# Kernel tuning notes

Measured on AMD Instinct MI355X. Metric: run time of the kernel, lower is better.

## Reference

```python
import jax, jax.numpy as jnp
import numpy as np

B, T, I, U, O, BB = 256, 1024, 64, 256, 64, 128  # batch, seq, input, units, output, backbone_units

def lecun_tanh(x):
    return 1.7159 * jnp.tanh(0.666 * x)

def setup_inputs() -> dict:
    key = jax.random.key(0)
    ks = jax.random.split(key, 13)
    def lin(k, fan_in, fan_out):
        bound = 1.0 / np.sqrt(fan_in)
        kw, kb = jax.random.split(k)
        W = jax.random.uniform(kw, (fan_in, fan_out), jnp.float32, -bound, bound)
        b = jax.random.uniform(kb, (fan_out,), jnp.float32, -bound, bound)
        return W, b
    x = jax.random.normal(ks[0], (B, T, I), jnp.float32)
    W_bb, b_bb = lin(ks[1], I + U, BB)   # backbone Linear
    W_ff1, b_ff1 = lin(ks[2], BB, U)
    W_ff2, b_ff2 = lin(ks[3], BB, U)
    W_ta, b_ta = lin(ks[4], BB, U)       # time_a
    W_tb, b_tb = lin(ks[5], BB, U)       # time_b
    W_fc, b_fc = lin(ks[6], U, O)        # readout
    return {"x": x, "W_bb": W_bb, "b_bb": b_bb, "W_ff1": W_ff1, "b_ff1": b_ff1,
            "W_ff2": W_ff2, "b_ff2": b_ff2, "W_ta": W_ta, "b_ta": b_ta,
            "W_tb": W_tb, "b_tb": b_tb, "W_fc": W_fc, "b_fc": b_fc}

def reference(x, W_bb, b_bb, W_ff1, b_ff1, W_ff2, b_ff2, W_ta, b_ta, W_tb, b_tb, W_fc, b_fc):
    ts = jnp.float32(1.0)  # default elapsed time per step
    def step(h, xt):
        z = jnp.concatenate([xt, h], axis=-1)          # [B, I+U]
        g = lecun_tanh(z @ W_bb + b_bb)                # [B, BB]
        ff1 = jnp.tanh(g @ W_ff1 + b_ff1)              # [B, U]
        ff2 = jnp.tanh(g @ W_ff2 + b_ff2)
        t_interp = jax.nn.sigmoid((g @ W_ta + b_ta) * ts + (g @ W_tb + b_tb))
        h_new = ff1 * (1.0 - t_interp) + t_interp * ff2
        return h_new, h_new
    h0 = jnp.zeros((x.shape[0], U), x.dtype)
    h_last, hs = jax.lax.scan(step, h0, jnp.swapaxes(x, 0, 1))  # hs: [T, B, U]
    hs = jnp.swapaxes(hs, 0, 1)                                  # [B, T, U]
    out = hs @ W_fc + b_fc                                       # [B, T, O]
    return out, h_last
```

## Files before the change

### kernel.cpp

```cpp
#include <hip/hip_runtime.h>
#include <stdint.h>

#define B_ 256
#define T_ 1024
#define I_ 64
#define U_ 256
#define O_ 64
#define BB_ 128

typedef unsigned int u32;
typedef unsigned short u16;
typedef _Float16 half2_t __attribute__((ext_vector_type(2)));
typedef _Float16 f16x8 __attribute__((ext_vector_type(8)));
typedef float f32x4 __attribute__((ext_vector_type(4)));

#if defined(__has_builtin)
#if __has_builtin(__builtin_amdgcn_fdot2)
#define USE_DOT2 1
#else
#define USE_DOT2 0
#endif
#else
#define USE_DOT2 0
#endif

static __device__ __forceinline__ u32 packpair(float a, float b) {
  half2_t h; h.x = (_Float16)a; h.y = (_Float16)b;
  return __builtin_bit_cast(u32, h);
}
static __device__ __forceinline__ float unpack_lo(u32 u) {
  half2_t h = __builtin_bit_cast(half2_t, u); return (float)h.x;
}
static __device__ __forceinline__ float unpack_hi(u32 u) {
  half2_t h = __builtin_bit_cast(half2_t, u); return (float)h.y;
}
static __device__ __forceinline__ float dot2acc(u32 w, u32 z, float acc) {
#if USE_DOT2
  return __builtin_amdgcn_fdot2(__builtin_bit_cast(half2_t, w),
                                __builtin_bit_cast(half2_t, z), acc, false);
#else
  half2_t hw = __builtin_bit_cast(half2_t, w);
  half2_t hz = __builtin_bit_cast(half2_t, z);
  acc += (float)hw.x * (float)hz.x;
  acc += (float)hw.y * (float)hz.y;
  return acc;
#endif
}

template <int CTRL>
static __device__ __forceinline__ float dpp_mov_f(float v) {
  return __builtin_bit_cast(float, __builtin_amdgcn_update_dpp(
      0, __builtin_bit_cast(int, v), CTRL, 0xF, 0xF, true));
}
#define DPP_XOR1 0xB1
#define DPP_XOR2 0x4E
#define DPP_HMIR 0x141
#define DPP_MIRR 0x140

static __device__ __forceinline__ float fast_tanh(float x) {
  return 1.0f - 2.0f / (1.0f + __expf(2.0f * x));
}
static __device__ __forceinline__ float fast_sigmoid(float x) {
  return 1.0f / (1.0f + __expf(-x));
}

static __device__ __forceinline__ float rcpf(float x) {
#if defined(__has_builtin) && __has_builtin(__builtin_amdgcn_rcpf)
  return __builtin_amdgcn_rcpf(x);
#else
  return 1.0f / x;
#endif
}
static __device__ __forceinline__ float exp2fast(float x) {
#if defined(__has_builtin) && __has_builtin(__builtin_amdgcn_exp2f)
  return __builtin_amdgcn_exp2f(x);
#else
  return exp2f(x);
#endif
}

static __device__ __forceinline__ f32x4 mfma16(uint4 a, uint4 b, f32x4 c) {
  return __builtin_amdgcn_mfma_f32_16x16x32_f16(
      __builtin_bit_cast(f16x8, a), __builtin_bit_cast(f16x8, b), c, 0, 0, 0);
}

#define LOG2E 1.44269504f

__global__ __launch_bounds__(512, 2)
void cfc_mfma(const float* __restrict__ x,
              const float* __restrict__ W_bb, const float* __restrict__ b_bb,
              const float* __restrict__ W_ff1, const float* __restrict__ b_ff1,
              const float* __restrict__ W_ff2, const float* __restrict__ b_ff2,
              const float* __restrict__ W_ta,  const float* __restrict__ b_ta,
              const float* __restrict__ W_tb,  const float* __restrict__ b_tb,
              float* __restrict__ out, u32* __restrict__ Hbuf)
{
  __shared__ __align__(16) u32 s_z[2560];
  __shared__ __align__(16) u32 s_g[1024];

  const int tid = threadIdx.x;
  const int l   = tid & 63;
  const int w   = tid >> 6;
  const int c16 = l & 15;
  const int q4  = l >> 4;
  const int odd = l & 1;
  const int row0 = blockIdx.x * 16;

  uint4 wbb[10];
  {
    const int colb = w * 16 + c16;
#pragma unroll
    for (int c = 0; c < 10; ++c) {
      u32 qv[4];
#pragma unroll
      for (int q = 0; q < 4; ++q) {
        const int k0 = c * 32 + q4 * 8 + 2 * q;
        qv[q] = packpair(W_bb[(size_t)k0 * BB_ + colb],
                         W_bb[(size_t)(k0 + 1) * BB_ + colb]);
      }
      wbb[c] = make_uint4(qv[0], qv[1], qv[2], qv[3]);
    }
  }
  uint4 wff[3][2][4];
#pragma unroll
  for (int ut = 0; ut < 2; ++ut) {
    const int u = w * 32 + ut * 16 + c16;
#pragma unroll
    for (int c = 0; c < 4; ++c) {
      u32 qa[4], qb[4], qc[4];
#pragma unroll
      for (int q = 0; q < 4; ++q) {
        const int k0 = c * 32 + q4 * 8 + 2 * q;
        const size_t i0 = (size_t)k0 * U_ + u, i1 = i0 + U_;
        qa[q] = packpair(W_ff1[i0], W_ff1[i1]);
        qb[q] = packpair(W_ff2[i0], W_ff2[i1]);
        qc[q] = packpair(W_ta[i0] + W_tb[i0], W_ta[i1] + W_tb[i1]);
      }
      wff[0][ut][c] = make_uint4(qa[0], qa[1], qa[2], qa[3]);
      wff[1][ut][c] = make_uint4(qb[0], qb[1], qb[2], qb[3]);
      wff[2][ut][c] = make_uint4(qc[0], qc[1], qc[2], qc[3]);
    }
  }

  const float bgs = b_bb[w * 16 + c16] * (1.332f * LOG2E);
  float b1s[2], b2s[2], btn[2];
#pragma unroll
  for (int ut = 0; ut < 2; ++ut) {
    const int u = w * 32 + ut * 16 + c16;
    b1s[ut] = b_ff1[u] * (2.0f * LOG2E);
    b2s[ut] = b_ff2[u] * (2.0f * LOG2E);
    btn[ut] = -(b_ta[u] + b_tb[u]) * LOG2E;
  }

  const int mx = tid >> 5, px = tid & 31;
  const float* xptr = x + (size_t)(row0 + mx) * T_ * I_ + 2 * px;
  const int zxw = ((px >> 4) * 64 + mx + 16 * ((px >> 2) & 3)) * 4 + (px & 3);

  const int rbase = odd ? 2 : 0;
  const int m0 = q4 * 4 + rbase, m1 = m0 + 1;
  const int pg = w * 8 + (c16 >> 1);
  const int gw0 = ((pg >> 4) * 64 + 16 * ((pg >> 2) & 3)) * 4 + (pg & 3)
                  + 16 * q4 + (odd ? 8 : 0);
  int zw_[2]; size_t hb0_[2], hb1_[2];
#pragma unroll
  for (int ut = 0; ut < 2; ++ut) {
    const int pu = w * 16 + ut * 8 + (c16 >> 1);
    zw_[ut] = ((2 + (pu >> 4)) * 64 + 16 * ((pu >> 2) & 3)) * 4 + (pu & 3)
              + 16 * q4 + (odd ? 8 : 0);
    hb0_[ut] = (size_t)(row0 + m0) * T_ * 128 + pu;
    hb1_[ut] = (size_t)(row0 + m1) * T_ * 128 + pu;
  }

  reinterpret_cast<uint4*>(s_z)[128 + tid] = make_uint4(0u, 0u, 0u, 0u);
  {
    float2 xv = *(const float2*)xptr;
    s_z[zxw] = packpair(xv.x, xv.y);
  }
  __syncthreads();

  const uint4* z4 = (const uint4*)s_z;
  const uint4* g4 = (const uint4*)s_g;

  for (int t = 0; t < T_; ++t) {
    float2 xv;
    const bool ldx = (t + 1 < T_);
    if (ldx) xv = *(const float2*)(xptr + (size_t)(t + 1) * I_);

    f32x4 aA = {0.f, 0.f, 0.f, 0.f}, aB = {0.f, 0.f, 0.f, 0.f};
#pragma unroll
    for (int c = 0; c < 10; c += 2) {
      aA = mfma16(z4[c * 64 + l],       wbb[c],     aA);
      aB = mfma16(z4[(c + 1) * 64 + l], wbb[c + 1], aB);
    }
    const f32x4 ab = aA + aB;

    u32 gq[4];
#pragma unroll
    for (int r = 0; r < 4; ++r) {
      const float a  = __builtin_fmaf(ab[r], 1.332f * LOG2E, bgs);
      const float rr = rcpf(exp2fast(a) + 1.0f);
      const float g  = __builtin_fmaf(rr, -3.4318f, 1.7159f);
      const float gp = dpp_mov_f<DPP_XOR1>(g);
      gq[r] = odd ? packpair(gp, g) : packpair(g, gp);
    }
    s_g[gw0]     = odd ? gq[2] : gq[0];
    s_g[gw0 + 4] = odd ? gq[3] : gq[1];
    __syncthreads();

    f32x4 af[3][2];
#pragma unroll
    for (int mt = 0; mt < 3; ++mt)
#pragma unroll
      for (int ut = 0; ut < 2; ++ut)
        af[mt][ut] = (f32x4){0.f, 0.f, 0.f, 0.f};
#pragma unroll
    for (int c = 0; c < 4; ++c) {
      const uint4 ga = g4[c * 64 + l];
#pragma unroll
      for (int mt = 0; mt < 3; ++mt)
#pragma unroll
        for (int ut = 0; ut < 2; ++ut)
          af[mt][ut] = mfma16(ga, wff[mt][ut][c], af[mt][ut]);
    }

#pragma unroll
    for (int ut = 0; ut < 2; ++ut) {
      u32 hq[4];
#pragma unroll
      for (int r = 0; r < 4; ++r) {
        const float a1 = __builtin_fmaf(af[0][ut][r], 2.0f * LOG2E, b1s[ut]);
        const float f1 = __builtin_fmaf(rcpf(exp2fast(a1) + 1.0f), -2.0f, 1.0f);
        const float a2 = __builtin_fmaf(af[1][ut][r], 2.0f * LOG2E, b2s[ut]);
        const float f2 = __builtin_fmaf(rcpf(exp2fast(a2) + 1.0f), -2.0f, 1.0f);
        const float at = __builtin_fmaf(af[2][ut][r], -LOG2E, btn[ut]);
        const float ti = rcpf(exp2fast(at) + 1.0f);
        const float h  = __builtin_fmaf(ti, f2 - f1, f1);
        const float hp = dpp_mov_f<DPP_XOR1>(h);
        hq[r] = odd ? packpair(hp, h) : packpair(h, hp);
      }
      const u32 s0 = odd ? hq[2] : hq[0];
      const u32 s1 = odd ? hq[3] : hq[1];
      s_z[zw_[ut]]     = s0;
      s_z[zw_[ut] + 4] = s1;
      Hbuf[hb0_[ut] + (size_t)t * 128] = s0;
      Hbuf[hb1_[ut] + (size_t)t * 128] = s1;
    }
    if (ldx) s_z[zxw] = packpair(xv.x, xv.y);
    __syncthreads();
  }

  {
    const uint4 hv = reinterpret_cast<const uint4*>(s_z)[128 + tid];
    float2* tail = (float2*)(out + (size_t)B_ * T_ * O_);
#pragma unroll
    for (int i = 0; i < 4; ++i) {
      const int vh   = tid * 4 + i;
      const int ch   = vh >> 8;
      const int lane = (vh >> 2) & 63;
      const int slot = vh & 3;
      const int m    = lane & 15;
      const int bq   = lane >> 4;
      const int pu   = ch * 16 + bq * 4 + slot;
      const u32 hp   = (i == 0) ? hv.x : (i == 1) ? hv.y : (i == 2) ? hv.z : hv.w;
      float2 hf; hf.x = unpack_lo(hp); hf.y = unpack_hi(hp);
      tail[(size_t)(row0 + m) * 128 + pu] = hf;
    }
  }
}

template <bool DEFER>
__global__ __launch_bounds__(1024)
void cfc_kernel(const float* __restrict__ x,
                const float* __restrict__ W_bb, const float* __restrict__ b_bb,
                const float* __restrict__ W_ff1, const float* __restrict__ b_ff1,
                const float* __restrict__ W_ff2, const float* __restrict__ b_ff2,
                const float* __restrict__ W_ta,  const float* __restrict__ b_ta,
                const float* __restrict__ W_tb,  const float* __restrict__ b_tb,
                const float* __restrict__ W_fc,  const float* __restrict__ b_fc,
                float* __restrict__ out, u32* __restrict__ Hbuf)
{
  __shared__ __align__(16) u32 s_z2[160];
  __shared__ __align__(16) u32 s_g2[64];
  u16* s_gh = (u16*)s_g2;

  const int tid = threadIdx.x;
  const int r   = blockIdx.x;

  const int ca  = tid >> 3;
  const int kga = tid & 7;
  const int jb = tid >> 2;
  const int kq = tid & 3;
  const int ro = tid >> 4;
  const int rk = tid & 15;

  u32 wbb[20];
#pragma unroll
  for (int j = 0; j < 5; ++j)
#pragma unroll
    for (int q = 0; q < 4; ++q) {
      int p = 4 * (kga + 8 * j) + q;
      wbb[4 * j + q] = packpair(W_bb[(2 * p) * BB_ + ca],
                                W_bb[(2 * p + 1) * BB_ + ca]);
    }
  u32 wf1[16], wf2[16], wta[16], wtb[16];
#pragma unroll
  for (int j = 0; j < 4; ++j)
#pragma unroll
    for (int q = 0; q < 4; ++q) {
      int p = 4 * (kq + 4 * j) + q;
      int k0 = 2 * p, k1 = 2 * p + 1;
      wf1[4 * j + q] = packpair(W_ff1[k0 * U_ + jb], W_ff1[k1 * U_ + jb]);
      wf2[4 * j + q] = packpair(W_ff2[k0 * U_ + jb], W_ff2[k1 * U_ + jb]);
      wta[4 * j + q] = packpair(W_ta [k0 * U_ + jb], W_ta [k1 * U_ + jb]);
      wtb[4 * j + q] = packpair(W_tb [k0 * U_ + jb], W_tb [k1 * U_ + jb]);
    }
  u32 wfc[8];
  float bfo = 0.f;
  if (!DEFER) {
#pragma unroll
    for (int j = 0; j < 2; ++j)
#pragma unroll
      for (int q = 0; q < 4; ++q) {
        int p = 4 * (rk + 16 * j) + q;
        wfc[4 * j + q] = packpair(W_fc[(2 * p) * O_ + ro],
                                  W_fc[(2 * p + 1) * O_ + ro]);
      }
    bfo = b_fc[ro];
  }
  const float bbbc = b_bb[ca];
  const float b1 = b_ff1[jb], b2 = b_ff2[jb];
  const float bta = b_ta[jb], btb = b_tb[jb];

  const float* xrow = x + (size_t)r * T_ * I_;
  const size_t out_row = (size_t)r * T_ * O_;
  u32* __restrict__ hrow = DEFER ? (Hbuf + (size_t)r * T_ * (U_ / 2)) : nullptr;

  if (tid < 160) s_z2[tid] = 0u;
  __syncthreads();
  if (tid < 32) {
    float2 xv = ((const float2*)xrow)[tid];
    s_z2[tid] = packpair(xv.x, xv.y);
  }
  __syncthreads();

  for (int t = 0; t < T_; ++t) {
    float2 xv;
    const bool ldx = (tid < 32) && (t + 1 < T_);
    if (ldx) xv = ((const float2*)(xrow + (size_t)(t + 1) * I_))[tid];

    float bacc = 0.f;
#pragma unroll
    for (int j = 0; j < 5; ++j) {
      uint4 zz = *reinterpret_cast<const uint4*>(s_z2 + 4 * (kga + 8 * j));
      bacc = dot2acc(wbb[4 * j + 0], zz.x, bacc);
      bacc = dot2acc(wbb[4 * j + 1], zz.y, bacc);
      bacc = dot2acc(wbb[4 * j + 2], zz.z, bacc);
      bacc = dot2acc(wbb[4 * j + 3], zz.w, bacc);
    }
    bacc += dpp_mov_f<DPP_XOR1>(bacc);
    bacc += dpp_mov_f<DPP_XOR2>(bacc);
    bacc += dpp_mov_f<DPP_HMIR>(bacc);
    float g = 1.7159f * fast_tanh(0.666f * (bacc + bbbc));

    float racc = 0.f;
    if (!DEFER) {
#pragma unroll
      for (int j = 0; j < 2; ++j) {
        uint4 hh = *reinterpret_cast<const uint4*>(s_z2 + 32 + 4 * (rk + 16 * j));
        racc = dot2acc(wfc[4 * j + 0], hh.x, racc);
        racc = dot2acc(wfc[4 * j + 1], hh.y, racc);
        racc = dot2acc(wfc[4 * j + 2], hh.z, racc);
        racc = dot2acc(wfc[4 * j + 3], hh.w, racc);
      }
      racc += dpp_mov_f<DPP_XOR1>(racc);
      racc += dpp_mov_f<DPP_XOR2>(racc);
      racc += dpp_mov_f<DPP_HMIR>(racc);
      racc += dpp_mov_f<DPP_MIRR>(racc);
    }
    if ((tid & 7) == 0)
      s_gh[ca] = __builtin_bit_cast(u16, (_Float16)g);
    if (!DEFER && t > 0 && rk == 0)
      out[out_row + (size_t)(t - 1) * O_ + ro] = racc + bfo;
    __syncthreads();

    float a1 = 0.f, a2 = 0.f, a3 = 0.f, a4 = 0.f;
#pragma unroll
    for (int j = 0; j < 4; ++j) {
      uint4 gg = *reinterpret_cast<const uint4*>(s_g2 + 4 * (kq + 4 * j));
      a1 = dot2acc(wf1[4 * j + 0], gg.x, a1);
      a1 = dot2acc(wf1[4 * j + 1], gg.y, a1);
      a1 = dot2acc(wf1[4 * j + 2], gg.z, a1);
      a1 = dot2acc(wf1[4 * j + 3], gg.w, a1);
      a2 = dot2acc(wf2[4 * j + 0], gg.x, a2);
      a2 = dot2acc(wf2[4 * j + 1], gg.y, a2);
      a2 = dot2acc(wf2[4 * j + 2], gg.z, a2);
      a2 = dot2acc(wf2[4 * j + 3], gg.w, a2);
      a3 = dot2acc(wta[4 * j + 0], gg.x, a3);
      a3 = dot2acc(wta[4 * j + 1], gg.y, a3);
      a3 = dot2acc(wta[4 * j + 2], gg.z, a3);
      a3 = dot2acc(wta[4 * j + 3], gg.w, a3);
      a4 = dot2acc(wtb[4 * j + 0], gg.x, a4);
      a4 = dot2acc(wtb[4 * j + 1], gg.y, a4);
      a4 = dot2acc(wtb[4 * j + 2], gg.z, a4);
      a4 = dot2acc(wtb[4 * j + 3], gg.w, a4);
    }
    a1 += dpp_mov_f<DPP_XOR1>(a1); a1 += dpp_mov_f<DPP_XOR2>(a1);
    a2 += dpp_mov_f<DPP_XOR1>(a2); a2 += dpp_mov_f<DPP_XOR2>(a2);
    a3 += dpp_mov_f<DPP_XOR1>(a3); a3 += dpp_mov_f<DPP_XOR2>(a3);
    a4 += dpp_mov_f<DPP_XOR1>(a4); a4 += dpp_mov_f<DPP_XOR2>(a4);
    float f1 = fast_tanh(a1 + b1);
    float f2 = fast_tanh(a2 + b2);
    float ti = fast_sigmoid(a3 + bta + a4 + btb);
    float h  = f1 + ti * (f2 - f1);
    float hq = dpp_mov_f<DPP_HMIR>(h);

    if ((tid & 7) == 0) {
      u32 pr = packpair(h, hq);
      int m = tid >> 3;
      s_z2[32 + m] = pr;
      if (DEFER) hrow[(size_t)t * (U_ / 2) + m] = pr;
    }
    if (ldx) s_z2[tid] = packpair(xv.x, xv.y);
    __syncthreads();
  }

  if (!DEFER) {
    float racc = 0.f;
#pragma unroll
    for (int j = 0; j < 2; ++j) {
      uint4 hh = *reinterpret_cast<const uint4*>(s_z2 + 32 + 4 * (rk + 16 * j));
      racc = dot2acc(wfc[4 * j + 0], hh.x, racc);
      racc = dot2acc(wfc[4 * j + 1], hh.y, racc);
      racc = dot2acc(wfc[4 * j + 2], hh.z, racc);
      racc = dot2acc(wfc[4 * j + 3], hh.w, racc);
    }
    racc += dpp_mov_f<DPP_XOR1>(racc);
    racc += dpp_mov_f<DPP_XOR2>(racc);
    racc += dpp_mov_f<DPP_HMIR>(racc);
    racc += dpp_mov_f<DPP_MIRR>(racc);
    if (rk == 0)
      out[out_row + (size_t)(T_ - 1) * O_ + ro] = racc + bfo;
  }

  if (tid < 128) {
    u32 hp = s_z2[32 + tid];
    float2 hv; hv.x = unpack_lo(hp); hv.y = unpack_hi(hp);
    ((float2*)(out + (size_t)B_ * T_ * O_))[r * 128 + tid] = hv;
  }
}

__global__ __launch_bounds__(512)
void ro_kernel(const u32* __restrict__ Hbuf,
               const float* __restrict__ W_fc, const float* __restrict__ b_fc,
               float* __restrict__ out)
{
  __shared__ __align__(16) u32 s_h[8 * 128];
  const int tid = threadIdx.x;
  const int o   = tid & 63;
  const int w   = tid >> 6;
  const int r   = blockIdx.x;

  u32 wfc[128];
#pragma unroll
  for (int p = 0; p < 128; ++p)
    wfc[p] = packpair(W_fc[(2 * p) * O_ + o], W_fc[(2 * p + 1) * O_ + o]);
  const float bo = b_fc[o];

  const u32* hrow = Hbuf + (size_t)r * T_ * 128;
  const size_t out_row = (size_t)r * T_ * O_;

  for (int c = 0; c < T_ / 8; ++c) {
    *(uint2*)(s_h + 2 * tid) =
        *(const uint2*)(hrow + (size_t)c * 1024 + 2 * tid);
    __syncthreads();
    float acc = bo;
    const uint4* h4 = reinterpret_cast<const uint4*>(s_h + w * 128);
#pragma unroll
    for (int i = 0; i < 32; ++i) {
      uint4 hh = h4[i];
      acc = dot2acc(wfc[4 * i + 0], hh.x, acc);
      acc = dot2acc(wfc[4 * i + 1], hh.y, acc);
      acc = dot2acc(wfc[4 * i + 2], hh.z, acc);
      acc = dot2acc(wfc[4 * i + 3], hh.w, acc);
    }
    out[out_row + (size_t)(8 * c + w) * O_ + o] = acc;
    __syncthreads();
  }
}

extern "C" void kernel_launch(void* const* d_in, const int* in_sizes, int n_in,
                              void* d_out, int out_size, void* d_ws, size_t ws_size,
                              hipStream_t stream) {
  const float* x     = (const float*)d_in[0];
  const float* W_bb  = (const float*)d_in[1];
  const float* b_bb  = (const float*)d_in[2];
  const float* W_ff1 = (const float*)d_in[3];
  const float* b_ff1 = (const float*)d_in[4];
  const float* W_ff2 = (const float*)d_in[5];
  const float* b_ff2 = (const float*)d_in[6];
  const float* W_ta  = (const float*)d_in[7];
  const float* b_ta  = (const float*)d_in[8];
  const float* W_tb  = (const float*)d_in[9];
  const float* b_tb  = (const float*)d_in[10];
  const float* W_fc  = (const float*)d_in[11];
  const float* b_fc  = (const float*)d_in[12];
  float* out = (float*)d_out;

  const size_t h_bytes = (size_t)B_ * T_ * (U_ / 2) * sizeof(u32);
  if (ws_size >= h_bytes) {
    u32* Hbuf = (u32*)d_ws;
    cfc_mfma<<<dim3(B_ / 16), dim3(512), 0, stream>>>(
        x, W_bb, b_bb, W_ff1, b_ff1, W_ff2, b_ff2,
        W_ta, b_ta, W_tb, b_tb, out, Hbuf);
    ro_kernel<<<dim3(B_), dim3(512), 0, stream>>>(Hbuf, W_fc, b_fc, out);
  } else {
    cfc_kernel<false><<<dim3(B_), dim3(1024), 0, stream>>>(
        x, W_bb, b_bb, W_ff1, b_ff1, W_ff2, b_ff2,
        W_ta, b_ta, W_tb, b_tb, W_fc, b_fc, out, nullptr);
  }
}
```

Before: 1.831 ms.

## Swizzle LDS layout for z/g tiles and use lightweight LDS-only barriers

Applies an XOR swizzle to the shared-memory layout of the z and g operand tiles, with matching read lane permutation, to reduce LDS bank conflicts on the scalar writes and vector MFMA operand reads. It also replaces __syncthreads in the time loop with a barrier that waits only on LDS counters, so outstanding global H stores and x prefetch loads no longer stall each recurrence step. The swizzle requires zeroing the whole z buffer up front, and correctness depends on global loads not being needed before the barrier.

```diff
diff --git a/kernel.cpp b/kernel.cpp
--- a/kernel.cpp
+++ b/kernel.cpp
@@ -84,6 +84,14 @@
       __builtin_bit_cast(f16x8, a), __builtin_bit_cast(f16x8, b), c, 0, 0, 0);
 }
 
+static __device__ __forceinline__ void wg_barrier() {
+  asm volatile("s_waitcnt lgkmcnt(0)\n\ts_barrier" ::: "memory");
+}
+
+static __device__ __forceinline__ int swzw(int w) {
+  return w ^ ((w >> 4) & 4);
+}
+
 #define LOG2E 1.44269504f
 
 __global__ __launch_bounds__(512, 2)
@@ -105,6 +113,7 @@
   const int q4  = l >> 4;
   const int odd = l & 1;
   const int row0 = blockIdx.x * 16;
+  const int lr = l ^ ((l >> 4) & 1);
 
   uint4 wbb[10];
   {
@@ -154,27 +163,35 @@
 
   const int mx = tid >> 5, px = tid & 31;
   const float* xptr = x + (size_t)(row0 + mx) * T_ * I_ + 2 * px;
-  const int zxw = ((px >> 4) * 64 + mx + 16 * ((px >> 2) & 3)) * 4 + (px & 3);
+  const int zxs = swzw(((px >> 4) * 64 + mx + 16 * ((px >> 2) & 3)) * 4 + (px & 3));
 
   const int rbase = odd ? 2 : 0;
   const int m0 = q4 * 4 + rbase, m1 = m0 + 1;
   const int pg = w * 8 + (c16 >> 1);
-  const int gw0 = ((pg >> 4) * 64 + 16 * ((pg >> 2) & 3)) * 4 + (pg & 3)
-                  + 16 * q4 + (odd ? 8 : 0);
-  int zw_[2]; size_t hb0_[2], hb1_[2];
+  const int gW = ((pg >> 4) * 64 + 16 * ((pg >> 2) & 3)) * 4 + (pg & 3)
+                 + 16 * q4 + (odd ? 8 : 0);
+  const int gws0 = swzw(gW), gws1 = swzw(gW + 4);
+  int zws0_[2], zws1_[2]; size_t hb0_[2], hb1_[2];
 #pragma unroll
   for (int ut = 0; ut < 2; ++ut) {
     const int pu = w * 16 + ut * 8 + (c16 >> 1);
-    zw_[ut] = ((2 + (pu >> 4)) * 64 + 16 * ((pu >> 2) & 3)) * 4 + (pu & 3)
-              + 16 * q4 + (odd ? 8 : 0);
+    const int zW = ((2 + (pu >> 4)) * 64 + 16 * ((pu >> 2) & 3)) * 4 + (pu & 3)
+                   + 16 * q4 + (odd ? 8 : 0);
+    zws0_[ut] = swzw(zW);
+    zws1_[ut] = swzw(zW + 4);
     hb0_[ut] = (size_t)(row0 + m0) * T_ * 128 + pu;
     hb1_[ut] = (size_t)(row0 + m1) * T_ * 128 + pu;
   }
 
-  reinterpret_cast<uint4*>(s_z)[128 + tid] = make_uint4(0u, 0u, 0u, 0u);
+  {
+    uint4* z4w = reinterpret_cast<uint4*>(s_z);
+#pragma unroll
+    for (int i = tid; i < 640; i += 512) z4w[i] = make_uint4(0u, 0u, 0u, 0u);
+  }
+  __syncthreads();
   {
     float2 xv = *(const float2*)xptr;
-    s_z[zxw] = packpair(xv.x, xv.y);
+    s_z[zxs] = packpair(xv.x, xv.y);
   }
   __syncthreads();
 
@@ -189,8 +206,8 @@
     f32x4 aA = {0.f, 0.f, 0.f, 0.f}, aB = {0.f, 0.f, 0.f, 0.f};
 #pragma unroll
     for (int c = 0; c < 10; c += 2) {
-      aA = mfma16(z4[c * 64 + l],       wbb[c],     aA);
-      aB = mfma16(z4[(c + 1) * 64 + l], wbb[c + 1], aB);
+      aA = mfma16(z4[c * 64 + lr],       wbb[c],     aA);
+      aB = mfma16(z4[(c + 1) * 64 + lr], wbb[c + 1], aB);
     }
     const f32x4 ab = aA + aB;
 
@@ -203,9 +220,9 @@
       const float gp = dpp_mov_f<DPP_XOR1>(g);
       gq[r] = odd ? packpair(gp, g) : packpair(g, gp);
     }
-    s_g[gw0]     = odd ? gq[2] : gq[0];
-    s_g[gw0 + 4] = odd ? gq[3] : gq[1];
-    __syncthreads();
+    s_g[gws0] = odd ? gq[2] : gq[0];
+    s_g[gws1] = odd ? gq[3] : gq[1];
+    wg_barrier();
 
     f32x4 af[3][2];
 #pragma unroll
@@ -215,7 +232,7 @@
         af[mt][ut] = (f32x4){0.f, 0.f, 0.f, 0.f};
 #pragma unroll
     for (int c = 0; c < 4; ++c) {
-      const uint4 ga = g4[c * 64 + l];
+      const uint4 ga = g4[c * 64 + lr];
 #pragma unroll
       for (int mt = 0; mt < 3; ++mt)
 #pragma unroll
@@ -240,17 +257,17 @@
       }
       const u32 s0 = odd ? hq[2] : hq[0];
       const u32 s1 = odd ? hq[3] : hq[1];
-      s_z[zw_[ut]]     = s0;
-      s_z[zw_[ut] + 4] = s1;
+      s_z[zws0_[ut]] = s0;
+      s_z[zws1_[ut]] = s1;
       Hbuf[hb0_[ut] + (size_t)t * 128] = s0;
       Hbuf[hb1_[ut] + (size_t)t * 128] = s1;
     }
-    if (ldx) s_z[zxw] = packpair(xv.x, xv.y);
-    __syncthreads();
+    if (ldx) s_z[zxs] = packpair(xv.x, xv.y);
+    wg_barrier();
   }
 
   {
-    const uint4 hv = reinterpret_cast<const uint4*>(s_z)[128 + tid];
+    const uint4 hv = z4[128 + (tid ^ ((tid >> 4) & 1))];
     float2* tail = (float2*)(out + (size_t)B_ * T_ * O_);
 #pragma unroll
     for (int i = 0; i < 4; ++i) {
```

New measurement: 1.946 ms. 6.2% more time.

## Precompute input projection in parallel kernel and fuse gate reciprocals

Applied to the files above, without the earlier changes.

Adds a parallel kernel that computes the x-part of the backbone projection plus bias for all timesteps into a workspace buffer. The recurrent kernel then does only the h-part MFMAs per step and loads the precomputed partial sum. The CfC output combination is also rewritten to use a single reciprocal instead of three. The cost is extra workspace, an extra launch and global traffic, half precision storage of the preactivation, and possible overflow in the combined product of exponentials.

```diff
diff --git a/kernel.cpp b/kernel.cpp
--- a/kernel.cpp
+++ b/kernel.cpp
@@ -87,13 +87,70 @@
 #define LOG2E 1.44269504f
 
 __global__ __launch_bounds__(512, 2)
+void px_kernel(const float* __restrict__ x,
+               const float* __restrict__ W_bb, const float* __restrict__ b_bb,
+               u32* __restrict__ Px)
+{
+  const int tid = threadIdx.x;
+  const int l   = tid & 63;
+  const int w   = tid >> 6;
+  const int c16 = l & 15;
+  const int q4  = l >> 4;
+  const int rr  = blockIdx.x;
+  const int t0  = blockIdx.y * 64;
+
+  uint4 wpx[2];
+  {
+    const int colb = w * 16 + c16;
+#pragma unroll
+    for (int c = 0; c < 2; ++c) {
+      u32 qv[4];
+#pragma unroll
+      for (int q = 0; q < 4; ++q) {
+        const int k0 = c * 32 + q4 * 8 + 2 * q;
+        qv[q] = packpair(W_bb[(size_t)k0 * BB_ + colb],
+                         W_bb[(size_t)(k0 + 1) * BB_ + colb]);
+      }
+      wpx[c] = make_uint4(qv[0], qv[1], qv[2], qv[3]);
+    }
+  }
+  const float bc = b_bb[w * 16 + c16];
+
+  const float* xr = x + ((size_t)(rr * 16 + c16)) * T_ * I_ + q4 * 8;
+  uint2* __restrict__ pxo =
+      (uint2*)Px + ((size_t)rr * T_ + t0) * 512 + w * 64 + l;
+
+  for (int i = 0; i < 64; ++i) {
+    const int t = t0 + i;
+    const float* xt = xr + (size_t)t * I_;
+    float4 v0 = *(const float4*)(xt);
+    float4 v1 = *(const float4*)(xt + 4);
+    float4 v2 = *(const float4*)(xt + 32);
+    float4 v3 = *(const float4*)(xt + 36);
+    uint4 a0 = make_uint4(packpair(v0.x, v0.y), packpair(v0.z, v0.w),
+                          packpair(v1.x, v1.y), packpair(v1.z, v1.w));
+    uint4 a1 = make_uint4(packpair(v2.x, v2.y), packpair(v2.z, v2.w),
+                          packpair(v3.x, v3.y), packpair(v3.z, v3.w));
+    f32x4 acc = {bc, bc, bc, bc};
+    acc = mfma16(a0, wpx[0], acc);
+    acc = mfma16(a1, wpx[1], acc);
+    uint2 o;
+    o.x = packpair(acc[0], acc[1]);
+    o.y = packpair(acc[2], acc[3]);
+    pxo[(size_t)i * 512] = o;
+  }
+}
+
+template <bool PX>
+__global__ __launch_bounds__(512, 2)
 void cfc_mfma(const float* __restrict__ x,
               const float* __restrict__ W_bb, const float* __restrict__ b_bb,
               const float* __restrict__ W_ff1, const float* __restrict__ b_ff1,
               const float* __restrict__ W_ff2, const float* __restrict__ b_ff2,
               const float* __restrict__ W_ta,  const float* __restrict__ b_ta,
               const float* __restrict__ W_tb,  const float* __restrict__ b_tb,
-              float* __restrict__ out, u32* __restrict__ Hbuf)
+              float* __restrict__ out, u32* __restrict__ Hbuf,
+              const u32* __restrict__ Px)
 {
   __shared__ __align__(16) u32 s_z[2560];
   __shared__ __align__(16) u32 s_g[1024];
@@ -104,17 +161,19 @@
   const int c16 = l & 15;
   const int q4  = l >> 4;
   const int odd = l & 1;
-  const int row0 = blockIdx.x * 16;
-
+  const int rr  = blockIdx.x;
+  const int row0 = rr * 16;
+
+  const int NBB = PX ? 8 : 10;
+  const int KOFF = PX ? 64 : 0;
   uint4 wbb[10];
   {
     const int colb = w * 16 + c16;
-#pragma unroll
-    for (int c = 0; c < 10; ++c) {
+    for (int c = 0; c < NBB; ++c) {
       u32 qv[4];
 #pragma unroll
       for (int q = 0; q < 4; ++q) {
-        const int k0 = c * 32 + q4 * 8 + 2 * q;
+        const int k0 = KOFF + c * 32 + q4 * 8 + 2 * q;
         qv[q] = packpair(W_bb[(size_t)k0 * BB_ + colb],
                          W_bb[(size_t)(k0 + 1) * BB_ + colb]);
       }
@@ -142,7 +201,7 @@
     }
   }
 
-  const float bgs = b_bb[w * 16 + c16] * (1.332f * LOG2E);
+  const float bgs = PX ? 0.f : b_bb[w * 16 + c16] * (1.332f * LOG2E);
   float b1s[2], b2s[2], btn[2];
 #pragma unroll
   for (int ut = 0; ut < 2; ++ut) {
@@ -152,9 +211,11 @@
     btn[ut] = -(b_ta[u] + b_tb[u]) * LOG2E;
   }
 
-  const int mx = tid >> 5, px = tid & 31;
-  const float* xptr = x + (size_t)(row0 + mx) * T_ * I_ + 2 * px;
-  const int zxw = ((px >> 4) * 64 + mx + 16 * ((px >> 2) & 3)) * 4 + (px & 3);
+  const int mx = tid >> 5, px_ = tid & 31;
+  const float* xptr = x + (size_t)(row0 + mx) * T_ * I_ + 2 * px_;
+  const int zxw = ((px_ >> 4) * 64 + mx + 16 * ((px_ >> 2) & 3)) * 4 + (px_ & 3);
+
+  const uint2* pxp = (const uint2*)Px + (size_t)rr * T_ * 512 + w * 64 + l;
 
   const int rbase = odd ? 2 : 0;
   const int m0 = q4 * 4 + rbase, m1 = m0 + 1;
@@ -172,7 +233,11 @@
   }
 
   reinterpret_cast<uint4*>(s_z)[128 + tid] = make_uint4(0u, 0u, 0u, 0u);
-  {
+  uint2 pxc;
+  if (PX) {
+    pxc = pxp[0];
+  } else {
+    __syncthreads();
     float2 xv = *(const float2*)xptr;
     s_z[zxw] = packpair(xv.x, xv.y);
   }
@@ -182,15 +247,34 @@
   const uint4* g4 = (const uint4*)s_g;
 
   for (int t = 0; t < T_; ++t) {
+    uint2 pxn;
     float2 xv;
-    const bool ldx = (t + 1 < T_);
-    if (ldx) xv = *(const float2*)(xptr + (size_t)(t + 1) * I_);
-
-    f32x4 aA = {0.f, 0.f, 0.f, 0.f}, aB = {0.f, 0.f, 0.f, 0.f};
-#pragma unroll
-    for (int c = 0; c < 10; c += 2) {
-      aA = mfma16(z4[c * 64 + l],       wbb[c],     aA);
-      aB = mfma16(z4[(c + 1) * 64 + l], wbb[c + 1], aB);
+    const bool more = (t + 1 < T_);
+    if (PX) {
+      if (more) pxn = pxp[(size_t)(t + 1) * 512];
+    } else {
+      if (more) xv = *(const float2*)(xptr + (size_t)(t + 1) * I_);
+    }
+
+    f32x4 aA, aB = {0.f, 0.f, 0.f, 0.f};
+    if (PX) {
+      aA = (f32x4){unpack_lo(pxc.x), unpack_hi(pxc.x),
+                   unpack_lo(pxc.y), unpack_hi(pxc.y)};
+      aA = mfma16(z4[2 * 64 + l], wbb[0], aA);
+      aB = mfma16(z4[3 * 64 + l], wbb[1], aB);
+      aA = mfma16(z4[4 * 64 + l], wbb[2], aA);
+      aB = mfma16(z4[5 * 64 + l], wbb[3], aB);
+      aA = mfma16(z4[6 * 64 + l], wbb[4], aA);
+      aB = mfma16(z4[7 * 64 + l], wbb[5], aB);
+      aA = mfma16(z4[8 * 64 + l], wbb[6], aA);
+      aB = mfma16(z4[9 * 64 + l], wbb[7], aB);
+    } else {
+      aA = (f32x4){0.f, 0.f, 0.f, 0.f};
+#pragma unroll
+      for (int c = 0; c < 10; c += 2) {
+        aA = mfma16(z4[c * 64 + l],       wbb[c],     aA);
+        aB = mfma16(z4[(c + 1) * 64 + l], wbb[c + 1], aB);
+      }
     }
     const f32x4 ab = aA + aB;
 
@@ -198,8 +282,8 @@
 #pragma unroll
     for (int r = 0; r < 4; ++r) {
       const float a  = __builtin_fmaf(ab[r], 1.332f * LOG2E, bgs);
-      const float rr = rcpf(exp2fast(a) + 1.0f);
-      const float g  = __builtin_fmaf(rr, -3.4318f, 1.7159f);
+      const float rv = rcpf(exp2fast(a) + 1.0f);
+      const float g  = __builtin_fmaf(rv, -3.4318f, 1.7159f);
       const float gp = dpp_mov_f<DPP_XOR1>(g);
       gq[r] = odd ? packpair(gp, g) : packpair(g, gp);
     }
@@ -228,13 +312,15 @@
       u32 hq[4];
 #pragma unroll
       for (int r = 0; r < 4; ++r) {
-        const float a1 = __builtin_fmaf(af[0][ut][r], 2.0f * LOG2E, b1s[ut]);
-        const float f1 = __builtin_fmaf(rcpf(exp2fast(a1) + 1.0f), -2.0f, 1.0f);
-        const float a2 = __builtin_fmaf(af[1][ut][r], 2.0f * LOG2E, b2s[ut]);
-        const float f2 = __builtin_fmaf(rcpf(exp2fast(a2) + 1.0f), -2.0f, 1.0f);
-        const float at = __builtin_fmaf(af[2][ut][r], -LOG2E, btn[ut]);
-        const float ti = rcpf(exp2fast(at) + 1.0f);
-        const float h  = __builtin_fmaf(ti, f2 - f1, f1);
+        const float E1 = exp2fast(__builtin_fmaf(af[0][ut][r], 2.0f * LOG2E, b1s[ut]));
+        const float E2 = exp2fast(__builtin_fmaf(af[1][ut][r], 2.0f * LOG2E, b2s[ut]));
+        const float E3 = exp2fast(__builtin_fmaf(af[2][ut][r], -LOG2E, btn[ut]));
+        const float p2 = E2 + 1.0f, p3 = E3 + 1.0f;
+        const float qq = p2 * p3;
+        const float D  = __builtin_fmaf(E1, qq, qq);
+        const float R  = rcpf(D);
+        const float u2 = (E2 - E1) - qq;
+        const float h  = __builtin_fmaf(R + R, u2, 1.0f);
         const float hp = dpp_mov_f<DPP_XOR1>(h);
         hq[r] = odd ? packpair(hp, h) : packpair(h, hp);
       }
@@ -245,7 +331,11 @@
       Hbuf[hb0_[ut] + (size_t)t * 128] = s0;
       Hbuf[hb1_[ut] + (size_t)t * 128] = s1;
     }
-    if (ldx) s_z[zxw] = packpair(xv.x, xv.y);
+    if (PX) {
+      pxc = pxn;
+    } else {
+      if (more) s_z[zxw] = packpair(xv.x, xv.y);
+    }
     __syncthreads();
   }
 
@@ -506,12 +596,21 @@
   const float* b_fc  = (const float*)d_in[12];
   float* out = (float*)d_out;
 
-  const size_t h_bytes = (size_t)B_ * T_ * (U_ / 2) * sizeof(u32);
-  if (ws_size >= h_bytes) {
+  const size_t h_bytes  = (size_t)B_ * T_ * (U_ / 2) * sizeof(u32);
+  const size_t px_bytes = (size_t)B_ * T_ * (BB_ / 2) * sizeof(u32);
+  if (ws_size >= h_bytes + px_bytes) {
     u32* Hbuf = (u32*)d_ws;
-    cfc_mfma<<<dim3(B_ / 16), dim3(512), 0, stream>>>(
+    u32* Px   = (u32*)((char*)d_ws + h_bytes);
+    px_kernel<<<dim3(16, T_ / 64), dim3(512), 0, stream>>>(x, W_bb, b_bb, Px);
+    cfc_mfma<true><<<dim3(B_ / 16), dim3(512), 0, stream>>>(
         x, W_bb, b_bb, W_ff1, b_ff1, W_ff2, b_ff2,
-        W_ta, b_ta, W_tb, b_tb, out, Hbuf);
+        W_ta, b_ta, W_tb, b_tb, out, Hbuf, Px);
+    ro_kernel<<<dim3(B_), dim3(512), 0, stream>>>(Hbuf, W_fc, b_fc, out);
+  } else if (ws_size >= h_bytes) {
+    u32* Hbuf = (u32*)d_ws;
+    cfc_mfma<false><<<dim3(B_ / 16), dim3(512), 0, stream>>>(
+        x, W_bb, b_bb, W_ff1, b_ff1, W_ff2, b_ff2,
+        W_ta, b_ta, W_tb, b_tb, out, Hbuf, nullptr);
     ro_kernel<<<dim3(B_), dim3(512), 0, stream>>>(Hbuf, W_fc, b_fc, out);
   } else {
     cfc_kernel<false><<<dim3(B_), dim3(1024), 0, stream>>>(
```

Measured after the change: 1.851 ms. Within noise of the previous version (+1.1%).
